# Optimization experiments

Hardware: AMD Instinct MI355X
Metric: run time of the kernel (lower is better)

## Reference

```python
import jax, jax.numpy as jnp
import numpy as np

B, P, C_IN, C = 2, 100000, 23, 64
H, W = 512, 512
S = H * W  # num voxels per batch element
EPS_BN1, EPS_BN2 = 1e-5, 1e-3


def setup_inputs() -> dict:
    key = jax.random.key(0)
    ks = jax.random.split(key, 16)
    valid = jax.random.uniform(ks[0], (B, P)) > 0.1
    inp = {
        "points_xyz": jax.random.normal(ks[1], (B, P, 3), jnp.float32),
        "points_feature": jax.random.normal(ks[2], (B, P, C_IN), jnp.float32),
        "points_mask": valid.astype(jnp.float32),
        "indices": jax.random.randint(ks[3], (B, P), 0, S, jnp.int32),
        "paddings": (1 - valid.astype(jnp.int32)),
        "voxel_xyz": jax.random.uniform(ks[4], (B, P, 3), jnp.float32) * 511.0,
        # PointNet linear (bias=False) + BatchNorm1d params (eval-style stats)
        "w_pn": jax.random.normal(ks[5], (C_IN, C), jnp.float32) * 0.1,
        "bn1_gamma": jax.random.uniform(ks[6], (C,), jnp.float32, 0.5, 1.5),
        "bn1_beta": jax.random.normal(ks[7], (C,), jnp.float32) * 0.1,
        "bn1_mean": jax.random.normal(ks[8], (C,), jnp.float32) * 0.1,
        "bn1_var": jax.random.uniform(ks[9], (C,), jnp.float32, 0.5, 1.5),
        # res1: Conv2d 1x1 (bias=False) + BatchNorm2d
        "conv_w": jax.random.normal(ks[10], (C, C), jnp.float32) * 0.05,  # [out,in]
        "bn2_gamma": jax.random.uniform(ks[11], (C,), jnp.float32, 0.5, 1.5),
        "bn2_beta": jax.random.normal(ks[12], (C,), jnp.float32) * 0.1,
        "bn2_mean": jax.random.normal(ks[13], (C,), jnp.float32) * 0.1,
        "bn2_var": jax.random.uniform(ks[14], (C,), jnp.float32, 0.5, 1.5),
    }
    return inp


def reference(points_xyz, points_feature, points_mask, indices, paddings, voxel_xyz,
              w_pn, bn1_gamma, bn1_beta, bn1_mean, bn1_var,
              conv_w, bn2_gamma, bn2_beta, bn2_mean, bn2_var):
    # ---- PointNet: Linear -> BN -> ReLU -> mask ----
    x = jnp.einsum("bpi,io->bpo", points_feature, w_pn)
    x = (x - bn1_mean) * jax.lax.rsqrt(bn1_var + EPS_BN1) * bn1_gamma + bn1_beta
    x = jax.nn.relu(x) * points_mask[..., None]  # [B,P,C]

    # ---- batched unsorted segment max (padded points -> dummy segment) ----
    valid = paddings == 0
    batch_off = jnp.arange(B, dtype=jnp.int32)[:, None] * S
    flat_ids = jnp.where(valid, indices + batch_off, B * S).reshape(-1)
    voxels = jax.ops.segment_max(x.reshape(B * P, C), flat_ids,
                                 num_segments=B * S + 1)[: B * S]
    voxels = jnp.where(jnp.isneginf(voxels), 0.0, voxels)  # empty voxels -> 0
    v = voxels.reshape(B, H, W, C)

    # ---- res1: 1x1 conv + BN + ReLU (NHWC layout) ----
    v = jnp.einsum("bhwc,oc->bhwo", v, conv_w)
    v = (v - bn2_mean) * jax.lax.rsqrt(bn2_var + EPS_BN2) * bn2_gamma + bn2_beta
    v = jax.nn.relu(v)

    # torch: voxels[B,C,H,W].permute(0,3,2,1) -> [B,W,H,C]; x indexes W, y indexes H
    im = jnp.transpose(v, (0, 2, 1, 3))  # [B,W,H,C]

    # ---- bilinear gather at voxel_xyz[..., :2] ----
    xq = voxel_xyz[..., 0]
    yq = voxel_xyz[..., 1]
    x0 = jnp.clip(jnp.floor(xq).astype(jnp.int32), 0, W - 1)
    x1 = jnp.clip(x0 + 1, 0, W - 1)
    y0 = jnp.clip(jnp.floor(yq).astype(jnp.int32), 0, H - 1)
    y1 = jnp.clip(y0 + 1, 0, H - 1)
    bidx = jnp.arange(B, dtype=jnp.int32)[:, None]
    Ia = im[bidx, x0, y0]
    Ib = im[bidx, x0, y1]
    Ic = im[bidx, x1, y0]
    Id = im[bidx, x1, y1]
    x0f, x1f = x0.astype(xq.dtype), x1.astype(xq.dtype)
    y0f, y1f = y0.astype(yq.dtype), y1.astype(yq.dtype)
    wa = (x1f - xq) * (y1f - yq)
    wb = (x1f - xq) * (yq - y0f)
    wc = (xq - x0f) * (y1f - yq)
    wd = (xq - x0f) * (yq - y0f)
    points_out = (wa[..., None] * Ia + wb[..., None] * Ib
                  + wc[..., None] * Ic + wd[..., None] * Id)  # [B,P,C]
    return points_out
```

## Files before the change

### kernel.cpp

```cpp
#include <hip/hip_runtime.h>
#include <hip/hip_bf16.h>

#define B_ 2
#define P_ 100000
#define CIN_ 23
#define C_ 64
#define H_ 512
#define W_ 512
#define S_ (H_*W_)
#define NPT_ (B_*P_)
#define NVOX_ (B_*S_)

typedef __attribute__((ext_vector_type(8))) short short8;
typedef __attribute__((ext_vector_type(4))) float f32x4;
typedef __attribute__((ext_vector_type(4))) int i32x4;
typedef __attribute__((ext_vector_type(4), aligned(4))) float f32x4u;

__device__ inline unsigned short f2bf(float f) {
    union { __hip_bfloat16 h; unsigned short u; } cv;
    cv.h = __float2bfloat16(f);
    return cv.u;
}
__device__ inline float bf2f(unsigned short u) {
    union { unsigned int i; float f; } cv;
    cv.i = ((unsigned int)u) << 16;
    return cv.f;
}
__device__ inline void bf2x(unsigned int u, float& lo, float& hi) {
    union { unsigned int i; float f; } a, b;
    a.i = u << 16;
    b.i = u & 0xffff0000u;
    lo = a.f; hi = b.f;
}

__global__ __launch_bounds__(256) void k_clear(int* __restrict__ cnt)
{
    int i = (blockIdx.x * 256 + threadIdx.x) * 4;
    if (i > NVOX_) return;
    *(i32x4*)(cnt + i) = (i32x4){0, 0, 0, 0};
}

__global__ __launch_bounds__(256) void k_hist(
    const int* __restrict__ indices,
    const int* __restrict__ paddings,
    int* __restrict__ cnt)
{
    int t4 = (blockIdx.x * 256 + threadIdx.x) * 4;
    if (t4 >= NPT_) return;
    i32x4 idx4 = *(const i32x4*)(indices + t4);
    i32x4 pad4 = *(const i32x4*)(paddings + t4);
    int vb = (t4 / P_) * S_;
    #pragma unroll
    for (int j = 0; j < 4; ++j)
        if (pad4[j] == 0) atomicAdd(&cnt[vb + idx4[j]], 1);
}

__global__ __launch_bounds__(256) void k_offsets(
    const int* __restrict__ cnt,
    int* __restrict__ off,
    int* __restrict__ cur,
    int* __restrict__ rid,
    int* __restrict__ off_c,
    int* __restrict__ cnt_c,
    int* __restrict__ gcursor,
    const float* __restrict__ conv_w,
    const float* __restrict__ w_pn,
    const float* __restrict__ g1, const float* __restrict__ b1,
    const float* __restrict__ m1, const float* __restrict__ v1,
    const float* __restrict__ g2, const float* __restrict__ b2,
    const float* __restrict__ m2, const float* __restrict__ v2,
    unsigned short* __restrict__ cwb,
    unsigned short* __restrict__ wpb,
    float* __restrict__ o1v,
    float* __restrict__ scv, float* __restrict__ shv)
{
    if (blockIdx.x >= 512) {
        int t = threadIdx.x;
        if (t < 64) {
            float s = g1[t] * rsqrtf(v1[t] + 1e-5f);
            o1v[t] = b1[t] - m1[t] * s;
            float s2 = g2[t] * rsqrtf(v2[t] + 1e-3f);
            scv[t] = s2;
            shv[t] = b2[t] - m2[t] * s2;
        }
        #pragma unroll
        for (int e = 0; e < 16; ++e) {
            int idx  = t * 16 + e;
            int f    = idx >> 9;
            int lane = (idx >> 3) & 63;
            int j    = idx & 7;
            int tq = f >> 1, ks = f & 1;
            int row = lane & 15, grp = lane >> 4;
            cwb[idx] = f2bf(conv_w[(tq * 16 + row) * 64 + ks * 32 + grp * 8 + j]);
        }
        #pragma unroll
        for (int e = 0; e < 8; ++e) {
            int idx  = t * 8 + e;
            int tq   = idx >> 9;
            int lane = (idx >> 3) & 63;
            int j    = idx & 7;
            int row = lane & 15, grp = lane >> 4;
            int n = tq * 16 + row;
            int k = grp * 8 + j;
            float s1n = g1[n] * rsqrtf(v1[n] + 1e-5f);
            wpb[idx] = (k < CIN_) ? f2bf(w_pn[k * C_ + n] * s1n) : 0;
        }
        return;
    }

    __shared__ int lds_c[256], lds_o[256];
    __shared__ int sbase_c, sbase_o;
    int tid  = threadIdx.x;
    int base = blockIdx.x * 1024 + tid * 4;
    i32x4 c = *(const i32x4*)(cnt + base);
    int o0 = c[0] > 0, o1 = c[1] > 0, o2 = c[2] > 0, o3 = c[3] > 0;
    int sc1 = c[0] + c[1], sc2 = sc1 + c[2], sc3 = sc2 + c[3];
    int so1 = o0 + o1,     so2 = so1 + o2,   so3 = so2 + o3;
    lds_c[tid] = sc3;
    lds_o[tid] = so3;
    __syncthreads();
    #pragma unroll
    for (int d = 1; d < 256; d <<= 1) {
        int vc = (tid >= d) ? lds_c[tid - d] : 0;
        int vo = (tid >= d) ? lds_o[tid - d] : 0;
        __syncthreads();
        if (tid >= d) { lds_c[tid] += vc; lds_o[tid] += vo; }
        __syncthreads();
    }
    if (tid == 0) {
        sbase_c = atomicAdd(&gcursor[0], lds_c[255]);
        sbase_o = atomicAdd(&gcursor[1], lds_o[255]);
    }
    __syncthreads();
    int oc = sbase_c + (tid == 0 ? 0 : lds_c[tid - 1]);
    int oo = sbase_o + (tid == 0 ? 0 : lds_o[tid - 1]);
    i32x4 e, ridv;
    e[0] = oc; e[1] = oc + c[0]; e[2] = oc + sc1; e[3] = oc + sc2;
    ridv[0] = o0 ? oo            : -1;
    ridv[1] = o1 ? oo + so1 - o1 : -1;
    ridv[2] = o2 ? oo + so2 - o2 : -1;
    ridv[3] = o3 ? oo + so3 - o3 : -1;
    *(i32x4*)(off + base) = e;
    *(i32x4*)(cur + base) = e;
    *(i32x4*)(rid + base) = ridv;
    #pragma unroll
    for (int i = 0; i < 4; ++i) {
        if (ridv[i] >= 0) {
            off_c[ridv[i]] = e[i];
            cnt_c[ridv[i]] = c[i];
        }
    }
}

__global__ __launch_bounds__(256) void k_z(
    const float* __restrict__ feat,
    const int* __restrict__ indices,
    const int* __restrict__ paddings,
    const unsigned short* __restrict__ wpb,
    int* __restrict__ cur,
    unsigned short* __restrict__ zs)
{
    int lane = threadIdx.x & 63;
    int wid  = (blockIdx.x * 256 + threadIdx.x) >> 6;
    int p0   = wid * 32;
    if (p0 >= NPT_) return;
    int row  = lane & 15;
    int grp  = lane >> 4;

    int slot = -1;
    if (lane < 32) {
        int pt = p0 + lane;
        if (paddings[pt] == 0) {
            int v = (pt / P_) * S_ + indices[pt];
            slot = atomicAdd(&cur[v], 1);
        }
    }

    const float* f0 = feat + (size_t)(p0 + row) * CIN_;
    const float* f1 = feat + (size_t)(p0 + 16 + row) * CIN_;
    short8 a0 = (short8){0,0,0,0,0,0,0,0};
    short8 a1 = (short8){0,0,0,0,0,0,0,0};
    if (grp < 3) {
        f32x4u u0 = *(const f32x4u*)(f0 + grp * 8);
        f32x4u u1 = *(const f32x4u*)(f0 + grp * 8 + 4);
        f32x4u w0 = *(const f32x4u*)(f1 + grp * 8);
        f32x4u w1 = *(const f32x4u*)(f1 + grp * 8 + 4);
        #pragma unroll
        for (int j = 0; j < 4; ++j) {
            int k0 = grp * 8 + j;
            int k1 = grp * 8 + 4 + j;
            a0[j]     = (short)(k0 < CIN_ ? f2bf(u0[j]) : 0);
            a0[j + 4] = (short)(k1 < CIN_ ? f2bf(u1[j]) : 0);
            a1[j]     = (short)(k0 < CIN_ ? f2bf(w0[j]) : 0);
            a1[j + 4] = (short)(k1 < CIN_ ? f2bf(w1[j]) : 0);
        }
    }

    short8 bfrag[4];
    #pragma unroll
    for (int t = 0; t < 4; ++t)
        bfrag[t] = *(const short8*)(wpb + ((size_t)t * 64 + lane) * 8);

    f32x4 acc0[4], acc1[4];
    #pragma unroll
    for (int t = 0; t < 4; ++t) {
        acc0[t] = (f32x4){0.f, 0.f, 0.f, 0.f};
        acc1[t] = (f32x4){0.f, 0.f, 0.f, 0.f};
    }
    #pragma unroll
    for (int t = 0; t < 4; ++t) {
        acc0[t] = __builtin_amdgcn_mfma_f32_16x16x32_bf16(a0, bfrag[t], acc0[t], 0, 0, 0);
        acc1[t] = __builtin_amdgcn_mfma_f32_16x16x32_bf16(a1, bfrag[t], acc1[t], 0, 0, 0);
    }

    #pragma unroll
    for (int r = 0; r < 4; ++r) {
        int sm0 = __shfl(slot, grp * 4 + r);
        int sm1 = __shfl(slot, 16 + grp * 4 + r);
        if (sm0 >= 0) {
            unsigned short* op = zs + (size_t)sm0 * C_;
            #pragma unroll
            for (int t = 0; t < 4; ++t)
                op[t * 16 + row] = f2bf(acc0[t][r]);
        }
        if (sm1 >= 0) {
            unsigned short* op = zs + (size_t)sm1 * C_;
            #pragma unroll
            for (int t = 0; t < 4; ++t)
                op[t * 16 + row] = f2bf(acc1[t][r]);
        }
    }
}

__global__ __launch_bounds__(256) void k_redconv(
    const unsigned short* __restrict__ zs,
    const int* __restrict__ off_c,
    const int* __restrict__ cnt_c,
    const int* __restrict__ gcursor,
    const float* __restrict__ o1v,
    const unsigned short* __restrict__ cwb,
    const float* __restrict__ scv, const float* __restrict__ shv,
    unsigned short* __restrict__ grid_c)
{
    int lane = threadIdx.x & 63;
    int wid  = (blockIdx.x * 256 + threadIdx.x) >> 6;
    int r0   = wid * 16;
    int nocc = gcursor[1];
    if (r0 >= nocc) return;

    int m    = lane & 15;
    int grp  = lane >> 4;
    int r    = r0 + m;
    bool liv = r < nocc;
    int ci = liv ? cnt_c[r] : 0;
    int oi = liv ? off_c[r] : 0;

    float mx[16];
    #pragma unroll
    for (int i = 0; i < 16; ++i) mx[i] = -1e30f;

    for (int j = 0; ; j += 2) {
        bool l0 = j < ci, l1 = (j + 1) < ci;
        if (!__any(l0)) break;
        const unsigned short* zr0 = zs + (size_t)(oi + (l0 ? j : 0)) * C_ + grp * 8;
        const unsigned short* zr1 = zs + (size_t)(oi + (l1 ? j + 1 : 0)) * C_ + grp * 8;
        short8 lo0 = *(const short8*)(zr0);
        short8 hi0 = *(const short8*)(zr0 + 32);
        short8 lo1 = *(const short8*)(zr1);
        short8 hi1 = *(const short8*)(zr1 + 32);
        if (l0) {
            #pragma unroll
            for (int jj = 0; jj < 8; ++jj) {
                mx[jj]     = fmaxf(mx[jj],     bf2f((unsigned short)lo0[jj]));
                mx[8 + jj] = fmaxf(mx[8 + jj], bf2f((unsigned short)hi0[jj]));
            }
        }
        if (l1) {
            #pragma unroll
            for (int jj = 0; jj < 8; ++jj) {
                mx[jj]     = fmaxf(mx[jj],     bf2f((unsigned short)lo1[jj]));
                mx[8 + jj] = fmaxf(mx[8 + jj], bf2f((unsigned short)hi1[jj]));
            }
        }
    }

    short8 a[2];
    #pragma unroll
    for (int jj = 0; jj < 8; ++jj) {
        int c0 = grp * 8 + jj;
        int c1 = 32 + grp * 8 + jj;
        a[0][jj] = (short)f2bf(fmaxf(mx[jj]     + o1v[c0], 0.f));
        a[1][jj] = (short)f2bf(fmaxf(mx[8 + jj] + o1v[c1], 0.f));
    }

    short8 bfrag[4][2];
    #pragma unroll
    for (int t = 0; t < 4; ++t)
        #pragma unroll
        for (int ks = 0; ks < 2; ++ks)
            bfrag[t][ks] = *(const short8*)(cwb + ((size_t)(t * 2 + ks) * 64 + lane) * 8);

    f32x4 acc[4];
    #pragma unroll
    for (int t = 0; t < 4; ++t) acc[t] = (f32x4){0.f, 0.f, 0.f, 0.f};
    #pragma unroll
    for (int t = 0; t < 4; ++t) {
        acc[t] = __builtin_amdgcn_mfma_f32_16x16x32_bf16(a[0], bfrag[t][0], acc[t], 0, 0, 0);
        acc[t] = __builtin_amdgcn_mfma_f32_16x16x32_bf16(a[1], bfrag[t][1], acc[t], 0, 0, 0);
    }

    float sc[4], sh[4];
    #pragma unroll
    for (int t = 0; t < 4; ++t) {
        int n = t * 16 + m;
        sc[t] = scv[n];
        sh[t] = shv[n];
    }
    #pragma unroll
    for (int rq = 0; rq < 4; ++rq) {
        int rr = r0 + grp * 4 + rq;
        if (rr < nocc) {
            unsigned short* op = grid_c + (size_t)rr * C_;
            #pragma unroll
            for (int t = 0; t < 4; ++t) {
                float val = fmaxf(acc[t][rq] * sc[t] + sh[t], 0.f);
                op[t * 16 + m] = f2bf(val);
            }
        }
    }
}

__global__ __launch_bounds__(256) void k_gather32(
    const unsigned short* __restrict__ grid_c,
    const int* __restrict__ rid,
    const float* __restrict__ vxyz,
    const float* __restrict__ shv,
    float* __restrict__ out)
{
    int lane = threadIdx.x & 63;
    int q    = lane >> 4;
    int ch   = (lane & 15) * 4;
    int gw   = (blockIdx.x * 256 + threadIdx.x) >> 6;
    int p0   = gw * 32;
    if (p0 >= NPT_) return;

    f32x4 cstv = *(const f32x4*)(shv + ch);
    #pragma unroll
    for (int j = 0; j < 4; ++j) cstv[j] = fmaxf(cstv[j], 0.f);

    const unsigned short* gc = grid_c + ch;

    #pragma unroll
    for (int it = 0; it < 8; ++it) {
        int pt = p0 + it * 4 + q;
        int b  = pt / P_;
        float xq = vxyz[(size_t)pt * 3 + 0];
        float yq = vxyz[(size_t)pt * 3 + 1];
        int x0 = (int)floorf(xq); x0 = min(max(x0, 0), W_ - 1);
        int x1 = min(x0 + 1, W_ - 1);
        int y0 = (int)floorf(yq); y0 = min(max(y0, 0), H_ - 1);
        int y1 = min(y0 + 1, H_ - 1);
        float x0f = (float)x0, x1f = (float)x1, y0f = (float)y0, y1f = (float)y1;
        float wa = (x1f - xq) * (y1f - yq);
        float wb = (x1f - xq) * (yq - y0f);
        float wc = (xq - x0f) * (y1f - yq);
        float wd = (xq - x0f) * (yq - y0f);

        int ia = y0 * W_ + x0, ib = y1 * W_ + x0, ic = y0 * W_ + x1, id = y1 * W_ + x1;
        const int* rb = rid + (size_t)b * S_;

        int ra = rb[ia], rbn = rb[ib], rc = rb[ic], rd = rb[id];
        uint2 Ra = *(const uint2*)(gc + (size_t)max(ra,  0) * C_);
        uint2 Rb = *(const uint2*)(gc + (size_t)max(rbn, 0) * C_);
        uint2 Rc = *(const uint2*)(gc + (size_t)max(rc,  0) * C_);
        uint2 Rd = *(const uint2*)(gc + (size_t)max(rd,  0) * C_);

        float A0,A1,A2,A3, B0,B1,B2,B3, C0,C1,C2,C3, D0,D1,D2,D3;
        bf2x(Ra.x, A0, A1); bf2x(Ra.y, A2, A3);
        bf2x(Rb.x, B0, B1); bf2x(Rb.y, B2, B3);
        bf2x(Rc.x, C0, C1); bf2x(Rc.y, C2, C3);
        bf2x(Rd.x, D0, D1); bf2x(Rd.y, D2, D3);

        bool oa = ra >= 0, ob = rbn >= 0, oc = rc >= 0, od = rd >= 0;
        f32x4 res;
        res[0] = wa * (oa ? A0 : cstv[0]) + wb * (ob ? B0 : cstv[0])
               + wc * (oc ? C0 : cstv[0]) + wd * (od ? D0 : cstv[0]);
        res[1] = wa * (oa ? A1 : cstv[1]) + wb * (ob ? B1 : cstv[1])
               + wc * (oc ? C1 : cstv[1]) + wd * (od ? D1 : cstv[1]);
        res[2] = wa * (oa ? A2 : cstv[2]) + wb * (ob ? B2 : cstv[2])
               + wc * (oc ? C2 : cstv[2]) + wd * (od ? D2 : cstv[2]);
        res[3] = wa * (oa ? A3 : cstv[3]) + wb * (ob ? B3 : cstv[3])
               + wc * (oc ? C3 : cstv[3]) + wd * (od ? D3 : cstv[3]);

        *(f32x4*)(out + (size_t)pt * C_ + ch) = res;
    }
}

extern "C" void kernel_launch(void* const* d_in, const int* in_sizes, int n_in,
                              void* d_out, int out_size, void* d_ws, size_t ws_size,
                              hipStream_t stream)
{
    const float* feat     = (const float*)d_in[1];
    const int*   indices  = (const int*)d_in[3];
    const int*   paddings = (const int*)d_in[4];
    const float* vxyz     = (const float*)d_in[5];
    const float* w_pn     = (const float*)d_in[6];
    const float* g1       = (const float*)d_in[7];
    const float* b1       = (const float*)d_in[8];
    const float* m1       = (const float*)d_in[9];
    const float* v1       = (const float*)d_in[10];
    const float* cw       = (const float*)d_in[11];
    const float* g2       = (const float*)d_in[12];
    const float* b2       = (const float*)d_in[13];
    const float* m2       = (const float*)d_in[14];
    const float* v2       = (const float*)d_in[15];

    char* p = (char*)d_ws;
    unsigned short* grid_c = (unsigned short*)p;  p += (size_t)NPT_ * C_ * 2;
    unsigned short* zs     = (unsigned short*)p;  p += (size_t)NPT_ * C_ * 2;
    int* cnt   = (int*)p;  p += (size_t)NVOX_ * 4;
    int* gcur  = (int*)p;  p += 16;
    int* off   = (int*)p;  p += (size_t)NVOX_ * 4;
    int* cur   = (int*)p;  p += (size_t)NVOX_ * 4;
    int* rid   = (int*)p;  p += (size_t)NVOX_ * 4;
    int* off_c = (int*)p;  p += (size_t)NPT_ * 4;
    int* cnt_c = (int*)p;  p += (size_t)NPT_ * 4;
    unsigned short* cwb = (unsigned short*)p;  p += 8 * 64 * 8 * 2;
    unsigned short* wpb = (unsigned short*)p;  p += 4 * 64 * 8 * 2;
    float* o1v = (float*)p;  p += 64 * 4;
    float* scv = (float*)p;  p += 64 * 4;
    float* shv = (float*)p;

    k_clear<<<513, 256, 0, stream>>>(cnt);

    k_hist<<<196, 256, 0, stream>>>(indices, paddings, cnt);

    k_offsets<<<513, 256, 0, stream>>>(cnt, off, cur, rid, off_c, cnt_c, gcur,
        cw, w_pn, g1, b1, m1, v1, g2, b2, m2, v2,
        cwb, wpb, o1v, scv, shv);

    k_z<<<1563, 256, 0, stream>>>(feat, indices, paddings, wpb, cur, zs);

    k_redconv<<<3125, 256, 0, stream>>>(zs, off_c, cnt_c, gcur, o1v, cwb, scv, shv, grid_c);

    k_gather32<<<1563, 256, 0, stream>>>(grid_c, rid, vxyz, shv, (float*)d_out);
}
```

Before: 83.79 us.

## Fuse PointNet matmul into segment-max kernel via sorted point-id permutation

Replaces the kernel that computed per-point bf16 features and scattered them into a sorted buffer with a lightweight kernel that only scatters point ids into sorted slots. The reduction kernel now gathers raw fp32 features through the id permutation, runs the 23->64 MFMA per segment member, and takes the running max in registers. It then stages the result through swizzled LDS to feed the conv MFMA. This drops the 25 MB intermediate write and read, at the cost of random gathers of the raw features and one MFMA per member iteration in a loop bounded by the wave's largest segment. The unused offset array write is also removed.

```diff
diff --git a/kernel.cpp b/kernel.cpp
--- a/kernel.cpp
+++ b/kernel.cpp
@@ -57,7 +57,6 @@
 
 __global__ __launch_bounds__(256) void k_offsets(
     const int* __restrict__ cnt,
-    int* __restrict__ off,
     int* __restrict__ cur,
     int* __restrict__ rid,
     int* __restrict__ off_c,
@@ -140,7 +139,6 @@
     ridv[1] = o1 ? oo + so1 - o1 : -1;
     ridv[2] = o2 ? oo + so2 - o2 : -1;
     ridv[3] = o3 ? oo + so3 - o3 : -1;
-    *(i32x4*)(off + base) = e;
     *(i32x4*)(cur + base) = e;
     *(i32x4*)(rid + base) = ridv;
     #pragma unroll
@@ -152,146 +150,104 @@
     }
 }
 
-__global__ __launch_bounds__(256) void k_z(
-    const float* __restrict__ feat,
+__global__ __launch_bounds__(256) void k_ptid(
     const int* __restrict__ indices,
     const int* __restrict__ paddings,
-    const unsigned short* __restrict__ wpb,
     int* __restrict__ cur,
-    unsigned short* __restrict__ zs)
-{
-    int lane = threadIdx.x & 63;
-    int wid  = (blockIdx.x * 256 + threadIdx.x) >> 6;
-    int p0   = wid * 32;
-    if (p0 >= NPT_) return;
-    int row  = lane & 15;
-    int grp  = lane >> 4;
-
-    int slot = -1;
-    if (lane < 32) {
-        int pt = p0 + lane;
-        if (paddings[pt] == 0) {
-            int v = (pt / P_) * S_ + indices[pt];
-            slot = atomicAdd(&cur[v], 1);
-        }
-    }
-
-    const float* f0 = feat + (size_t)(p0 + row) * CIN_;
-    const float* f1 = feat + (size_t)(p0 + 16 + row) * CIN_;
-    short8 a0 = (short8){0,0,0,0,0,0,0,0};
-    short8 a1 = (short8){0,0,0,0,0,0,0,0};
-    if (grp < 3) {
-        f32x4u u0 = *(const f32x4u*)(f0 + grp * 8);
-        f32x4u u1 = *(const f32x4u*)(f0 + grp * 8 + 4);
-        f32x4u w0 = *(const f32x4u*)(f1 + grp * 8);
-        f32x4u w1 = *(const f32x4u*)(f1 + grp * 8 + 4);
-        #pragma unroll
-        for (int j = 0; j < 4; ++j) {
-            int k0 = grp * 8 + j;
-            int k1 = grp * 8 + 4 + j;
-            a0[j]     = (short)(k0 < CIN_ ? f2bf(u0[j]) : 0);
-            a0[j + 4] = (short)(k1 < CIN_ ? f2bf(u1[j]) : 0);
-            a1[j]     = (short)(k0 < CIN_ ? f2bf(w0[j]) : 0);
-            a1[j + 4] = (short)(k1 < CIN_ ? f2bf(w1[j]) : 0);
-        }
-    }
-
-    short8 bfrag[4];
-    #pragma unroll
-    for (int t = 0; t < 4; ++t)
-        bfrag[t] = *(const short8*)(wpb + ((size_t)t * 64 + lane) * 8);
-
-    f32x4 acc0[4], acc1[4];
-    #pragma unroll
-    for (int t = 0; t < 4; ++t) {
-        acc0[t] = (f32x4){0.f, 0.f, 0.f, 0.f};
-        acc1[t] = (f32x4){0.f, 0.f, 0.f, 0.f};
-    }
-    #pragma unroll
-    for (int t = 0; t < 4; ++t) {
-        acc0[t] = __builtin_amdgcn_mfma_f32_16x16x32_bf16(a0, bfrag[t], acc0[t], 0, 0, 0);
-        acc1[t] = __builtin_amdgcn_mfma_f32_16x16x32_bf16(a1, bfrag[t], acc1[t], 0, 0, 0);
-    }
-
-    #pragma unroll
-    for (int r = 0; r < 4; ++r) {
-        int sm0 = __shfl(slot, grp * 4 + r);
-        int sm1 = __shfl(slot, 16 + grp * 4 + r);
-        if (sm0 >= 0) {
-            unsigned short* op = zs + (size_t)sm0 * C_;
-            #pragma unroll
-            for (int t = 0; t < 4; ++t)
-                op[t * 16 + row] = f2bf(acc0[t][r]);
-        }
-        if (sm1 >= 0) {
-            unsigned short* op = zs + (size_t)sm1 * C_;
-            #pragma unroll
-            for (int t = 0; t < 4; ++t)
-                op[t * 16 + row] = f2bf(acc1[t][r]);
-        }
-    }
+    int* __restrict__ ptid)
+{
+    int pt = blockIdx.x * 256 + threadIdx.x;
+    if (pt >= NPT_) return;
+    if (paddings[pt] != 0) return;
+    int v = (pt / P_) * S_ + indices[pt];
+    int slot = atomicAdd(&cur[v], 1);
+    ptid[slot] = pt;
 }
 
 __global__ __launch_bounds__(256) void k_redconv(
-    const unsigned short* __restrict__ zs,
+    const float* __restrict__ feat,
+    const int* __restrict__ ptid,
     const int* __restrict__ off_c,
     const int* __restrict__ cnt_c,
     const int* __restrict__ gcursor,
+    const unsigned short* __restrict__ wpb,
     const float* __restrict__ o1v,
     const unsigned short* __restrict__ cwb,
     const float* __restrict__ scv, const float* __restrict__ shv,
     unsigned short* __restrict__ grid_c)
 {
+    __shared__ unsigned short lds[4][16][64];
+
     int lane = threadIdx.x & 63;
+    int wv   = threadIdx.x >> 6;
     int wid  = (blockIdx.x * 256 + threadIdx.x) >> 6;
     int r0   = wid * 16;
     int nocc = gcursor[1];
     if (r0 >= nocc) return;
 
-    int m    = lane & 15;
-    int grp  = lane >> 4;
-    int r    = r0 + m;
-    bool liv = r < nocc;
-    int ci = liv ? cnt_c[r] : 0;
-    int oi = liv ? off_c[r] : 0;
-
-    float mx[16];
-    #pragma unroll
-    for (int i = 0; i < 16; ++i) mx[i] = -1e30f;
-
-    for (int j = 0; ; j += 2) {
-        bool l0 = j < ci, l1 = (j + 1) < ci;
-        if (!__any(l0)) break;
-        const unsigned short* zr0 = zs + (size_t)(oi + (l0 ? j : 0)) * C_ + grp * 8;
-        const unsigned short* zr1 = zs + (size_t)(oi + (l1 ? j + 1 : 0)) * C_ + grp * 8;
-        short8 lo0 = *(const short8*)(zr0);
-        short8 hi0 = *(const short8*)(zr0 + 32);
-        short8 lo1 = *(const short8*)(zr1);
-        short8 hi1 = *(const short8*)(zr1 + 32);
-        if (l0) {
+    int col = lane & 15;
+    int grp = lane >> 4;
+
+    int rA    = r0 + col;
+    bool livA = rA < nocc;
+    int ciA   = livA ? cnt_c[rA] : 0;
+    int oiA   = livA ? off_c[rA] : 0;
+
+    int ci4[4];
+    #pragma unroll
+    for (int r = 0; r < 4; ++r) ci4[r] = __shfl(ciA, grp * 4 + r);
+
+    short8 bz[4];
+    #pragma unroll
+    for (int t = 0; t < 4; ++t)
+        bz[t] = *(const short8*)(wpb + ((size_t)t * 64 + lane) * 8);
+
+    f32x4 mx[4];
+    #pragma unroll
+    for (int t = 0; t < 4; ++t) mx[t] = (f32x4){-1e30f, -1e30f, -1e30f, -1e30f};
+
+    for (int j = 0; ; ++j) {
+        if (!__any(j < ciA)) break;
+        int jj = j < ciA ? j : 0;
+        int pt = ptid[oiA + jj];
+        const float* f = feat + (size_t)pt * CIN_;
+        short8 a = (short8){0,0,0,0,0,0,0,0};
+        if (grp < 3) {
+            f32x4u v0 = *(const f32x4u*)(f + grp * 8);
+            f32x4u v1 = *(const f32x4u*)(f + grp * 8 + 4);
             #pragma unroll
-            for (int jj = 0; jj < 8; ++jj) {
-                mx[jj]     = fmaxf(mx[jj],     bf2f((unsigned short)lo0[jj]));
-                mx[8 + jj] = fmaxf(mx[8 + jj], bf2f((unsigned short)hi0[jj]));
+            for (int jx = 0; jx < 4; ++jx) {
+                int k0 = grp * 8 + jx;
+                int k1 = k0 + 4;
+                a[jx]     = (short)(k0 < CIN_ ? f2bf(v0[jx]) : 0);
+                a[jx + 4] = (short)(k1 < CIN_ ? f2bf(v1[jx]) : 0);
             }
         }
-        if (l1) {
+        #pragma unroll
+        for (int t = 0; t < 4; ++t) {
+            f32x4 zt = __builtin_amdgcn_mfma_f32_16x16x32_bf16(
+                a, bz[t], (f32x4){0.f, 0.f, 0.f, 0.f}, 0, 0, 0);
             #pragma unroll
-            for (int jj = 0; jj < 8; ++jj) {
-                mx[jj]     = fmaxf(mx[jj],     bf2f((unsigned short)lo1[jj]));
-                mx[8 + jj] = fmaxf(mx[8 + jj], bf2f((unsigned short)hi1[jj]));
-            }
-        }
-    }
-
-    short8 a[2];
-    #pragma unroll
-    for (int jj = 0; jj < 8; ++jj) {
-        int c0 = grp * 8 + jj;
-        int c1 = 32 + grp * 8 + jj;
-        a[0][jj] = (short)f2bf(fmaxf(mx[jj]     + o1v[c0], 0.f));
-        a[1][jj] = (short)f2bf(fmaxf(mx[8 + jj] + o1v[c1], 0.f));
-    }
+            for (int r = 0; r < 4; ++r)
+                if (j < ci4[r]) mx[t][r] = fmaxf(mx[t][r], zt[r]);
+        }
+    }
+
+    #pragma unroll
+    for (int t = 0; t < 4; ++t) {
+        float o1 = o1v[t * 16 + col];
+        #pragma unroll
+        for (int r = 0; r < 4; ++r) {
+            int row = grp * 4 + r;
+            float val = fmaxf(mx[t][r] + o1, 0.f);
+            lds[wv][row][(t * 16 + col) ^ ((row & 7) << 3)] = f2bf(val);
+        }
+    }
+
+    short8 a2[2];
+    #pragma unroll
+    for (int ks = 0; ks < 2; ++ks)
+        a2[ks] = *(const short8*)&lds[wv][col][(ks * 32 + grp * 8) ^ ((col & 7) << 3)];
 
     short8 bfrag[4][2];
     #pragma unroll
@@ -305,14 +261,14 @@
     for (int t = 0; t < 4; ++t) acc[t] = (f32x4){0.f, 0.f, 0.f, 0.f};
     #pragma unroll
     for (int t = 0; t < 4; ++t) {
-        acc[t] = __builtin_amdgcn_mfma_f32_16x16x32_bf16(a[0], bfrag[t][0], acc[t], 0, 0, 0);
-        acc[t] = __builtin_amdgcn_mfma_f32_16x16x32_bf16(a[1], bfrag[t][1], acc[t], 0, 0, 0);
+        acc[t] = __builtin_amdgcn_mfma_f32_16x16x32_bf16(a2[0], bfrag[t][0], acc[t], 0, 0, 0);
+        acc[t] = __builtin_amdgcn_mfma_f32_16x16x32_bf16(a2[1], bfrag[t][1], acc[t], 0, 0, 0);
     }
 
     float sc[4], sh[4];
     #pragma unroll
     for (int t = 0; t < 4; ++t) {
-        int n = t * 16 + m;
+        int n = t * 16 + col;
         sc[t] = scv[n];
         sh[t] = shv[n];
     }
@@ -324,7 +280,7 @@
             #pragma unroll
             for (int t = 0; t < 4; ++t) {
                 float val = fmaxf(acc[t][rq] * sc[t] + sh[t], 0.f);
-                op[t * 16 + m] = f2bf(val);
+                op[t * 16 + col] = f2bf(val);
             }
         }
     }
@@ -417,14 +373,13 @@
 
     char* p = (char*)d_ws;
     unsigned short* grid_c = (unsigned short*)p;  p += (size_t)NPT_ * C_ * 2;
-    unsigned short* zs     = (unsigned short*)p;  p += (size_t)NPT_ * C_ * 2;
     int* cnt   = (int*)p;  p += (size_t)NVOX_ * 4;
     int* gcur  = (int*)p;  p += 16;
-    int* off   = (int*)p;  p += (size_t)NVOX_ * 4;
     int* cur   = (int*)p;  p += (size_t)NVOX_ * 4;
     int* rid   = (int*)p;  p += (size_t)NVOX_ * 4;
     int* off_c = (int*)p;  p += (size_t)NPT_ * 4;
     int* cnt_c = (int*)p;  p += (size_t)NPT_ * 4;
+    int* ptid  = (int*)p;  p += (size_t)NPT_ * 4;
     unsigned short* cwb = (unsigned short*)p;  p += 8 * 64 * 8 * 2;
     unsigned short* wpb = (unsigned short*)p;  p += 4 * 64 * 8 * 2;
     float* o1v = (float*)p;  p += 64 * 4;
@@ -435,13 +390,14 @@
 
     k_hist<<<196, 256, 0, stream>>>(indices, paddings, cnt);
 
-    k_offsets<<<513, 256, 0, stream>>>(cnt, off, cur, rid, off_c, cnt_c, gcur,
+    k_offsets<<<513, 256, 0, stream>>>(cnt, cur, rid, off_c, cnt_c, gcur,
         cw, w_pn, g1, b1, m1, v1, g2, b2, m2, v2,
         cwb, wpb, o1v, scv, shv);
 
-    k_z<<<1563, 256, 0, stream>>>(feat, indices, paddings, wpb, cur, zs);
-
-    k_redconv<<<3125, 256, 0, stream>>>(zs, off_c, cnt_c, gcur, o1v, cwb, scv, shv, grid_c);
+    k_ptid<<<(NPT_ + 255) / 256, 256, 0, stream>>>(indices, paddings, cur, ptid);
+
+    k_redconv<<<3125, 256, 0, stream>>>(feat, ptid, off_c, cnt_c, gcur,
+        wpb, o1v, cwb, scv, shv, grid_c);
 
     k_gather32<<<1563, 256, 0, stream>>>(grid_c, rid, vxyz, shv, (float*)d_out);
 }
```

New measurement: 81.50 us. 2.7% less time.
